# Kernel tuning notes

Hardware: AMD Instinct MI355X
Metric: run time of the kernel (lower is better)

## Reference

```python
import jax, jax.numpy as jnp
import numpy as np

T, B, IN, H, OUT = 345, 128, 13, 128, 9

# snnTorch ATan surrogate spike: forward = heaviside(x), backward = 1/(1+(pi*x)^2) (alpha=2)
@jax.custom_vjp
def spike_fn(x):
    return (x > 0).astype(x.dtype)

def _spike_fwd(x):
    return spike_fn(x), x

def _spike_bwd(x, g):
    return (g / (1.0 + (jnp.pi * x) ** 2),)

spike_fn.defvjp(_spike_fwd, _spike_bwd)


def setup_inputs() -> dict:
    key = jax.random.key(0)
    ks = jax.random.split(key, 5)
    x = jax.random.normal(ks[0], (B, IN, T), dtype=jnp.float32)
    # PyTorch Linear init: U(-1/sqrt(fan_in), 1/sqrt(fan_in))
    lim1 = 1.0 / np.sqrt(IN)
    lim2 = 1.0 / np.sqrt(H)
    W1 = jax.random.uniform(ks[1], (H, IN), minval=-lim1, maxval=lim1, dtype=jnp.float32)
    b1 = jax.random.uniform(ks[2], (H,), minval=-lim1, maxval=lim1, dtype=jnp.float32)
    W2 = jax.random.uniform(ks[3], (OUT, H), minval=-lim2, maxval=lim2, dtype=jnp.float32)
    b2 = jax.random.uniform(ks[4], (OUT,), minval=-lim2, maxval=lim2, dtype=jnp.float32)
    beta1 = jnp.float32(0.9)
    thr1 = jnp.float32(1.0)
    beta2 = jnp.float32(0.9)
    thr2 = jnp.float32(1.0)
    return {"x": x, "W1": W1, "b1": b1, "W2": W2, "b2": b2,
            "beta1": beta1, "thr1": thr1, "beta2": beta2, "thr2": thr2}


def reference(x, W1, b1, W2, b2, beta1, thr1, beta2, thr2):
    # Precompute fc1 for all steps: (T, B, H)
    cur1_all = jnp.einsum('bct,hc->tbh', x, W1) + b1
    bt1 = jnp.clip(beta1, 0.0, 1.0)
    bt2 = jnp.clip(beta2, 0.0, 1.0)

    def step(carry, cur1):
        mem1, mem2 = carry
        mem1 = bt1 * mem1 + cur1                 # leaky integrate
        spk1 = spike_fn(mem1 - thr1)             # fire
        mem1 = mem1 - spk1 * thr1                # subtract reset
        cur2 = spk1 @ W2.T + b2                  # (B, OUT)
        mem2 = bt2 * mem2 + cur2
        spk2 = spike_fn(mem2 - thr2)
        mem2 = mem2 - spk2 * thr2
        return (mem1, mem2), (spk2, mem2)

    init = (jnp.zeros((B, H), x.dtype), jnp.zeros((B, OUT), x.dtype))
    _, (spk_rec, mem_rec) = jax.lax.scan(step, init, cur1_all)
    return spk_rec, mem_rec  # each (T, B, OUT)
```

## Files before the change

### kernel.cpp

```cpp
#include <hip/hip_runtime.h>

#define T_STEPS 345
#define B_SZ    128
#define IN_SZ   13
#define H_SZ    128
#define OUT_SZ  9
#define CPAD    388
#define NBO     (B_SZ * OUT_SZ)
#define CHUNK   92
#define BUFR    100


__device__ __forceinline__ void emit_cur1(float* __restrict__ buf,
                                          const float* __restrict__ xst,
                                          const float (&w1r)[4][IN_SZ],
                                          const float (&b1r)[4],
                                          int T0, int L, int hq, int off, int stride)
{
    for (int tl = off; tl < L; tl += stride) {
        const int t = T0 + tl;
        const float4* xq = (const float4*)(xst + t * 16);
        const float4 x0 = xq[0], x1 = xq[1], x2 = xq[2];
        const float x12 = xst[t * 16 + 12];
        const float xa[IN_SZ] = { x0.x,x0.y,x0.z,x0.w, x1.x,x1.y,x1.z,x1.w,
                                  x2.x,x2.y,x2.z,x2.w, x12 };
        float* brow = buf + tl * H_SZ + hq;
#pragma unroll
        for (int k2 = 0; k2 < 4; ++k2) {
            float cur = b1r[k2];
#pragma unroll
            for (int c = 0; c < IN_SZ; ++c) cur = fmaf(xa[c], w1r[k2][c], cur);
            brow[k2 * 32] = cur;
        }
    }
}

__device__ __forceinline__ void scan1_step(float& mem1, float u, float bt1, float th1,
                                           unsigned long long* __restrict__ msh,
                                           int t, bool sl, int half)
{
    mem1 = fmaf(bt1, mem1, u);
    const bool p = mem1 > th1;
    const unsigned long long m = __ballot(p);
    const float ms = mem1 - th1;
    mem1 = p ? ms : mem1;
    if (sl) msh[t * 2 + half] = m;
}

__device__ __forceinline__ void scan1_chunk(const float* __restrict__ buf,
                                            unsigned long long* __restrict__ msh,
                                            int T0, int L, int h,
                                            float bt1, float th1, float& mem1)
{
    const float* cb = buf + h;
    const bool sl = (h & 63) == 0;
    const int half = h >> 6;
    float a0 = cb[0*128], a1 = cb[1*128], a2 = cb[2*128], a3 = cb[3*128];
    float b0 = cb[4*128], b1v = cb[5*128], b2v = cb[6*128], b3 = cb[7*128];
    const int fullg = L >> 2;
    const int rem   = L & 3;
    for (int g = 0; g < fullg; ++g) {
        const float u0 = a0, u1 = a1, u2 = a2, u3 = a3;
        a0 = b0; a1 = b1v; a2 = b2v; a3 = b3;
        const float* nb = cb + (g + 2) * 4 * 128;
        b0 = nb[0]; b1v = nb[128]; b2v = nb[256]; b3 = nb[384];
        const int tb = T0 + g * 4;
        scan1_step(mem1, u0, bt1, th1, msh, tb + 0, sl, half);
        scan1_step(mem1, u1, bt1, th1, msh, tb + 1, sl, half);
        scan1_step(mem1, u2, bt1, th1, msh, tb + 2, sl, half);
        scan1_step(mem1, u3, bt1, th1, msh, tb + 3, sl, half);
    }
    const int tb = T0 + fullg * 4;
    if (rem > 0) scan1_step(mem1, a0, bt1, th1, msh, tb + 0, sl, half);
    if (rem > 1) scan1_step(mem1, a1, bt1, th1, msh, tb + 1, sl, half);
    if (rem > 2) scan1_step(mem1, a2, bt1, th1, msh, tb + 2, sl, half);
}

__global__ __launch_bounds__(512, 2)
void snn_fused(const float* __restrict__ x, const float* __restrict__ W1,
               const float* __restrict__ b1, const float* __restrict__ W2,
               const float* __restrict__ b2,
               const float* __restrict__ beta1p, const float* __restrict__ thr1p,
               const float* __restrict__ beta2p, const float* __restrict__ thr2p,
               float* __restrict__ out)
{
    const int b    = blockIdx.x >> 1;
    const int half = blockIdx.x & 1;
    const int tid  = threadIdx.x;
    const int wid  = tid >> 6;
    const int lane = tid & 63;

    __shared__ __align__(16) float xst[T_STEPS * 16];
    __shared__ __align__(16) float cur1s[2][BUFR * H_SZ];
    __shared__ __align__(16) unsigned long long msh[352 * 2];
    __shared__ __align__(16) float c2s[OUT_SZ * CPAD];

    const float* xb = x + (size_t)b * (IN_SZ * T_STEPS);
    for (int i = tid; i < IN_SZ * T_STEPS; i += 512) {
        const int c = i / T_STEPS;
        const int t = i - c * T_STEPS;
        xst[t * 16 + c] = xb[i];
    }
    float* W1t = c2s;
    for (int i = tid; i < IN_SZ * H_SZ; i += 512) {
        const int h = i / IN_SZ;
        const int c = i - IN_SZ * h;
        W1t[c * H_SZ + h] = W1[i];
    }
    __syncthreads();

    const int hq = tid & 31;
    float w1r[4][IN_SZ];
    float b1r[4];
#pragma unroll
    for (int k2 = 0; k2 < 4; ++k2) {
        b1r[k2] = b1[hq + 32 * k2];
#pragma unroll
        for (int c = 0; c < IN_SZ; ++c) w1r[k2][c] = W1t[c * H_SZ + hq + 32 * k2];
    }
    const float bt1 = fminf(fmaxf(beta1p[0], 0.0f), 1.0f);
    const float th1 = thr1p[0];

    emit_cur1(cur1s[0], xst, w1r, b1r, 0, CHUNK, hq, tid >> 5, 16);
    __syncthreads();

    float mem1 = 0.0f;
    for (int k = 0; k < 4; ++k) {
        if (tid < 128) {
            const int L = (k < 3) ? CHUNK : (T_STEPS - 3 * CHUNK);
            scan1_chunk(cur1s[k & 1], msh, k * CHUNK, L, tid, bt1, th1, mem1);
        } else if (k < 3) {
            const int kn = k + 1;
            const int L = (kn < 3) ? CHUNK : (T_STEPS - 3 * CHUNK);
            emit_cur1(cur1s[kn & 1], xst, w1r, b1r, kn * CHUNK, L, hq, (tid >> 5) - 4, 12);
        }
        __syncthreads();
    }

    const int obase  = half ? 5 : 0;
    const int ntasks = half ? 4 : 5;
    const float bt2 = fminf(fmaxf(beta2p[0], 0.0f), 1.0f);
    const float th2 = thr2p[0];

    float mem2 = 0.0f;
    const int o_sc = obase + lane;
    float* out_spk = out + (size_t)b * OUT_SZ + o_sc;
    float* out_mem = out_spk + (size_t)T_STEPS * NBO;
    const float4* src4 = (const float4*)(c2s + lane * CPAD);

    for (int s = 0; s < 6; ++s) {
        if (wid < 7) {
            if (wid < ntasks) {
                const int o = obase + wid;
                const int t = s * 64 + lane;
                const int tc = (t < T_STEPS) ? t : (T_STEPS - 1);
                const uint4 mm = *(const uint4*)((const char*)msh + (size_t)tc * 16);
                const float* __restrict__ w2row = W2 + o * H_SZ;
                float acc = 0.0f;
#pragma unroll
                for (int h = 0; h < 32; ++h)
                    acc = fmaf((float)((mm.x >> h) & 1u), w2row[h], acc);
#pragma unroll
                for (int h = 0; h < 32; ++h)
                    acc = fmaf((float)((mm.y >> h) & 1u), w2row[32 + h], acc);
#pragma unroll
                for (int h = 0; h < 32; ++h)
                    acc = fmaf((float)((mm.z >> h) & 1u), w2row[64 + h], acc);
#pragma unroll
                for (int h = 0; h < 32; ++h)
                    acc = fmaf((float)((mm.w >> h) & 1u), w2row[96 + h], acc);
                c2s[wid * CPAD + t] = acc + b2[o];
            }
        } else if (s > 0 && lane < ntasks) {
            const int sb = (s - 1) * 16;
            float4 fA = src4[sb], fB = src4[sb + 1];
#pragma unroll
            for (int i = 0; i < 16; ++i) {
                const float4 u = fA; fA = fB; fB = src4[sb + i + 2];
                const float vv[4] = { u.x, u.y, u.z, u.w };
#pragma unroll
                for (int kk = 0; kk < 4; ++kk) {
                    const int tt = (s - 1) * 64 + i * 4 + kk;
                    mem2 = fmaf(bt2, mem2, vv[kk]);
                    const bool p = mem2 > th2;
                    const float s2 = p ? 1.0f : 0.0f;
                    const float ms = mem2 - th2;
                    mem2 = p ? ms : mem2;
                    out_spk[(size_t)tt * NBO] = s2;
                    out_mem[(size_t)tt * NBO] = mem2;
                }
            }
        }
        __syncthreads();
    }

    if (wid == 7 && lane < ntasks) {
        const int sb = 5 * 16;
        float4 fA = src4[sb], fB = src4[sb + 1];
#pragma unroll
        for (int i = 0; i < 16; ++i) {
            const float4 u = fA; fA = fB; fB = src4[sb + i + 2];
            const float vv[4] = { u.x, u.y, u.z, u.w };
#pragma unroll
            for (int kk = 0; kk < 4; ++kk) {
                const int tt = 5 * 64 + i * 4 + kk;
                if (tt < T_STEPS) {
                    mem2 = fmaf(bt2, mem2, vv[kk]);
                    const bool p = mem2 > th2;
                    const float s2 = p ? 1.0f : 0.0f;
                    const float ms = mem2 - th2;
                    mem2 = p ? ms : mem2;
                    out_spk[(size_t)tt * NBO] = s2;
                    out_mem[(size_t)tt * NBO] = mem2;
                }
            }
        }
    }
}

extern "C" void kernel_launch(void* const* d_in, const int* in_sizes, int n_in,
                              void* d_out, int out_size, void* d_ws, size_t ws_size,
                              hipStream_t stream) {
    const float* x     = (const float*)d_in[0];
    const float* W1    = (const float*)d_in[1];
    const float* b1    = (const float*)d_in[2];
    const float* W2    = (const float*)d_in[3];
    const float* b2    = (const float*)d_in[4];
    const float* beta1 = (const float*)d_in[5];
    const float* thr1  = (const float*)d_in[6];
    const float* beta2 = (const float*)d_in[7];
    const float* thr2  = (const float*)d_in[8];
    float* out = (float*)d_out;
    (void)in_sizes; (void)n_in; (void)out_size; (void)d_ws; (void)ws_size;

    snn_fused<<<dim3(B_SZ * 2), dim3(512), 0, stream>>>(
        x, W1, b1, W2, b2, beta1, thr1, beta2, thr2, out);
}
```

Measured before the change: 103.7 us.

## Transpose x staging to channel-major and give each thread one hidden unit in cur1 emit

The shared-memory x buffer changes from time-major (t*16+c) to channel-major (c*XT+t). The fc1 producer is reworked so each thread owns a single hidden unit with 13 weights in registers instead of 4x13, and computes two timesteps per iteration. The scan's register prefetch pipeline is deepened from two groups of four rows to three, and the buffer row count grows to match. This lowers register pressure and spreads producer work differently, but it adds more scalar LDS reads of x per output and slightly more shared memory.

After: 107.8 us. +4.0%, slower.

```diff
diff --git a/kernel.cpp b/kernel.cpp
--- a/kernel.cpp
+++ b/kernel.cpp
@@ -5,33 +5,36 @@
 #define IN_SZ   13
 #define H_SZ    128
 #define OUT_SZ  9
+#define XT      348
 #define CPAD    388
 #define NBO     (B_SZ * OUT_SZ)
 #define CHUNK   92
-#define BUFR    100
-
-
-__device__ __forceinline__ void emit_cur1(float* __restrict__ buf,
-                                          const float* __restrict__ xst,
-                                          const float (&w1r)[4][IN_SZ],
-                                          const float (&b1r)[4],
-                                          int T0, int L, int hq, int off, int stride)
-{
-    for (int tl = off; tl < L; tl += stride) {
-        const int t = T0 + tl;
-        const float4* xq = (const float4*)(xst + t * 16);
-        const float4 x0 = xq[0], x1 = xq[1], x2 = xq[2];
-        const float x12 = xst[t * 16 + 12];
-        const float xa[IN_SZ] = { x0.x,x0.y,x0.z,x0.w, x1.x,x1.y,x1.z,x1.w,
-                                  x2.x,x2.y,x2.z,x2.w, x12 };
-        float* brow = buf + tl * H_SZ + hq;
-#pragma unroll
-        for (int k2 = 0; k2 < 4; ++k2) {
-            float cur = b1r[k2];
-#pragma unroll
-            for (int c = 0; c < IN_SZ; ++c) cur = fmaf(xa[c], w1r[k2][c], cur);
-            brow[k2 * 32] = cur;
-        }
+#define BUFR    104
+
+
+__device__ __forceinline__ void emit_rows(float* __restrict__ buf,
+                                          const float* __restrict__ xs,
+                                          const float (&w1r)[IN_SZ], float b1r,
+                                          int T0, int L, int h, int off, int stride)
+{
+    int tl = off;
+    for (; tl + stride < L; tl += 2 * stride) {
+        const int ta = T0 + tl, tb = T0 + tl + stride;
+        float ca = b1r, cb = b1r;
+#pragma unroll
+        for (int c = 0; c < IN_SZ; ++c) {
+            ca = fmaf(xs[c * XT + ta], w1r[c], ca);
+            cb = fmaf(xs[c * XT + tb], w1r[c], cb);
+        }
+        buf[tl * H_SZ + h] = ca;
+        buf[(tl + stride) * H_SZ + h] = cb;
+    }
+    if (tl < L) {
+        const int ta = T0 + tl;
+        float ca = b1r;
+#pragma unroll
+        for (int c = 0; c < IN_SZ; ++c) ca = fmaf(xs[c * XT + ta], w1r[c], ca);
+        buf[tl * H_SZ + h] = ca;
     }
 }
 
@@ -55,15 +58,17 @@
     const float* cb = buf + h;
     const bool sl = (h & 63) == 0;
     const int half = h >> 6;
-    float a0 = cb[0*128], a1 = cb[1*128], a2 = cb[2*128], a3 = cb[3*128];
-    float b0 = cb[4*128], b1v = cb[5*128], b2v = cb[6*128], b3 = cb[7*128];
+    float a0 = cb[0*128], a1 = cb[1*128], a2 = cb[ 2*128], a3 = cb[ 3*128];
+    float b0 = cb[4*128], b1v= cb[5*128], b2v= cb[ 6*128], b3 = cb[ 7*128];
+    float c0 = cb[8*128], c1v= cb[9*128], c2v= cb[10*128], c3 = cb[11*128];
     const int fullg = L >> 2;
     const int rem   = L & 3;
     for (int g = 0; g < fullg; ++g) {
         const float u0 = a0, u1 = a1, u2 = a2, u3 = a3;
         a0 = b0; a1 = b1v; a2 = b2v; a3 = b3;
-        const float* nb = cb + (g + 2) * 4 * 128;
-        b0 = nb[0]; b1v = nb[128]; b2v = nb[256]; b3 = nb[384];
+        b0 = c0; b1v = c1v; b2v = c2v; b3 = c3;
+        const float* nb = cb + (g + 3) * 4 * 128;
+        c0 = nb[0]; c1v = nb[128]; c2v = nb[256]; c3 = nb[384];
         const int tb = T0 + g * 4;
         scan1_step(mem1, u0, bt1, th1, msh, tb + 0, sl, half);
         scan1_step(mem1, u1, bt1, th1, msh, tb + 1, sl, half);
@@ -89,8 +94,10 @@
     const int tid  = threadIdx.x;
     const int wid  = tid >> 6;
     const int lane = tid & 63;
-
-    __shared__ __align__(16) float xst[T_STEPS * 16];
+    const int hown = tid & 127;
+    const int jsl  = tid >> 7;
+
+    __shared__ __align__(16) float xst[IN_SZ * XT];
     __shared__ __align__(16) float cur1s[2][BUFR * H_SZ];
     __shared__ __align__(16) unsigned long long msh[352 * 2];
     __shared__ __align__(16) float c2s[OUT_SZ * CPAD];
@@ -99,7 +106,7 @@
     for (int i = tid; i < IN_SZ * T_STEPS; i += 512) {
         const int c = i / T_STEPS;
         const int t = i - c * T_STEPS;
-        xst[t * 16 + c] = xb[i];
+        xst[c * XT + t] = xb[i];
     }
     float* W1t = c2s;
     for (int i = tid; i < IN_SZ * H_SZ; i += 512) {
@@ -109,19 +116,14 @@
     }
     __syncthreads();
 
-    const int hq = tid & 31;
-    float w1r[4][IN_SZ];
-    float b1r[4];
-#pragma unroll
-    for (int k2 = 0; k2 < 4; ++k2) {
-        b1r[k2] = b1[hq + 32 * k2];
-#pragma unroll
-        for (int c = 0; c < IN_SZ; ++c) w1r[k2][c] = W1t[c * H_SZ + hq + 32 * k2];
-    }
+    float w1r[IN_SZ];
+#pragma unroll
+    for (int c = 0; c < IN_SZ; ++c) w1r[c] = W1t[c * H_SZ + hown];
+    const float b1r = b1[hown];
     const float bt1 = fminf(fmaxf(beta1p[0], 0.0f), 1.0f);
     const float th1 = thr1p[0];
 
-    emit_cur1(cur1s[0], xst, w1r, b1r, 0, CHUNK, hq, tid >> 5, 16);
+    emit_rows(cur1s[0], xst, w1r, b1r, 0, CHUNK, hown, jsl, 4);
     __syncthreads();
 
     float mem1 = 0.0f;
@@ -132,7 +134,7 @@
         } else if (k < 3) {
             const int kn = k + 1;
             const int L = (kn < 3) ? CHUNK : (T_STEPS - 3 * CHUNK);
-            emit_cur1(cur1s[kn & 1], xst, w1r, b1r, kn * CHUNK, L, hq, (tid >> 5) - 4, 12);
+            emit_rows(cur1s[kn & 1], xst, w1r, b1r, kn * CHUNK, L, hown, jsl - 1, 3);
         }
         __syncthreads();
     }
```
